# Performance work log

Measured on AMD Instinct MI355X. Metric: run time of the kernel, lower is better.

The kernel has to match this reference:

```python
import jax, jax.numpy as jnp
import numpy as np

D_MODEL = 1024
N_HEADS = 16
HEAD_DIM = D_MODEL // N_HEADS
WINDOW = 256


def setup_inputs() -> dict:
    key = jax.random.key(0)
    kx, kq, ko = jax.random.split(key, 3)
    B, T = 4, 2048
    x = jax.random.normal(kx, (B, T, D_MODEL), dtype=jnp.float32)
    s = 1.0 / np.sqrt(D_MODEL)
    w_qkv = jax.random.normal(kq, (D_MODEL, 3 * D_MODEL), dtype=jnp.float32) * s
    w_out = jax.random.normal(ko, (D_MODEL, D_MODEL), dtype=jnp.float32) * s
    return {"x": x, "w_qkv": w_qkv, "w_out": w_out}


def reference(x, w_qkv, w_out):
    B, T, C = x.shape
    qkv = (x @ w_qkv).reshape(B, T, 3, N_HEADS, HEAD_DIM)
    q, k, v = qkv[:, :, 0], qkv[:, :, 1], qkv[:, :, 2]  # [B,T,H,D]
    # sliding-window causal mask: position i attends to j in (i-W, i]
    i = jnp.arange(T)[:, None]
    j = jnp.arange(T)[None, :]
    allowed = (j <= i) & (j > i - WINDOW)
    mask = jnp.where(allowed, 0.0, -jnp.inf).astype(x.dtype)  # [T,T]
    scale = 1.0 / np.sqrt(HEAD_DIM)
    scores = jnp.einsum('bqhd,bkhd->bhqk', q, k) * scale + mask
    attn = jax.nn.softmax(scores, axis=-1)
    out = jnp.einsum('bhqk,bkhd->bqhd', attn, v).reshape(B, T, C)
    return out @ w_out
```

## Files before the change

kernel.cpp:

```cpp
#include <hip/hip_runtime.h>

typedef unsigned short u16;
typedef __attribute__((ext_vector_type(8))) short bh8;
typedef __attribute__((ext_vector_type(4))) float f4;
typedef __attribute__((ext_vector_type(4))) unsigned short us4;

#define T_SEQ 2048
#define NHEADS 16
#define DHEAD 64
#define WIN 256

#define MF(a, b, c) __builtin_amdgcn_mfma_f32_16x16x32_bf16((a), (b), (c), 0, 0, 0)

__device__ __forceinline__ float bf2f(u16 u) {
  union { unsigned int i; float f; } v; v.i = ((unsigned int)u) << 16; return v.f;
}
__device__ __forceinline__ u16 f2bf(float f) {
  unsigned int u = __float_as_uint(f);
  u = u + 0x7fffu + ((u >> 16) & 1u);
  return (u16)(u >> 16);
}
__device__ __forceinline__ void async16(const void* g, void* l) {
  void* gv = const_cast<void*>(g);
  __builtin_amdgcn_global_load_lds(
      (__attribute__((address_space(1))) void*)gv,
      (__attribute__((address_space(3))) void*)l, 16, 0, 0);
}

__device__ __forceinline__ int is_f32_probe(const void* x) {
  const float* xf = (const float*)x;
  const int lane = threadIdx.x & 63;
  int bad = 0;
  #pragma unroll
  for (int u = 0; u < 4; ++u) {
    const float v = xf[lane * 4 + u];
    const float a = fabsf(v);
    bad |= (!(a < 64.f)) || (!(v == 0.f || a > 1e-30f));
  }
  return __any(bad) ? 0 : 1;
}

__global__ __launch_bounds__(256) void prep(
    const void* __restrict__ x, const void* __restrict__ w_qkv,
    const void* __restrict__ w_out, u16* __restrict__ xbf,
    u16* __restrict__ wqkvT, u16* __restrict__ woutT, int have_x)
{
  const int bid = blockIdx.x;
  const int tid = threadIdx.x;
  const int isf = is_f32_probe(x);

  if (bid < 4096) {
    if (!have_x) return;
    const size_t e = ((size_t)bid * 256 + tid) * 8;
    if (isf) {
      const float* f = (const float*)x;
      us4 o0, o1;
      #pragma unroll
      for (int u = 0; u < 4; ++u) { o0[u] = f2bf(f[e + u]); o1[u] = f2bf(f[e + 4 + u]); }
      *(us4*)&xbf[e] = o0; *(us4*)&xbf[e + 4] = o1;
    } else {
      *(us4*)&xbf[e]     = *(const us4*)&((const u16*)x)[e];
      *(us4*)&xbf[e + 4] = *(const us4*)&((const u16*)x)[e + 4];
    }
  } else {
    __shared__ alignas(16) u16 tile[32][33];
    const void* in; u16* out; int C, bx, by;
    const int t0 = bid - 4096;
    if (t0 < 3072) { in = w_qkv; out = wqkvT; C = 3072; bx = t0 % 96; by = t0 / 96; }
    else           { const int t = t0 - 3072; in = w_out; out = woutT; C = 1024; bx = t % 32; by = t / 32; }
    const int tx4 = (tid & 7) * 4;
    const int iy  = tid >> 3;
    const int y0 = by * 32;
    if (isf) {
      f4 v = *(const f4*)&((const float*)in)[(size_t)(y0 + iy) * C + bx * 32 + tx4];
      #pragma unroll
      for (int u = 0; u < 4; ++u) tile[iy][tx4 + u] = f2bf(v[u]);
    } else {
      us4 v = *(const us4*)&((const u16*)in)[(size_t)(y0 + iy) * C + bx * 32 + tx4];
      #pragma unroll
      for (int u = 0; u < 4; ++u) tile[iy][tx4 + u] = v[u];
    }
    __syncthreads();
    const int i2 = tid >> 3;
    us4 o;
    #pragma unroll
    for (int u = 0; u < 4; ++u) o[u] = tile[tx4 + u][i2];
    *(us4*)&out[(size_t)(bx * 32 + i2) * 1024 + y0 + tx4] = o;
  }
}

template<int BN, bool ADYN, bool CDYN>
__global__ __launch_bounds__(256, 4) void gemm_bt(
    const void* __restrict__ A, const u16* __restrict__ Bt,
    void* __restrict__ C, int N, int K, int lda, int ldc,
    const void* __restrict__ xprobe)
{
  constexpr int NJ = BN / 32;
  __shared__ alignas(16) u16 As[128 * 64];
  __shared__ alignas(16) u16 Bs[BN * 64];

  const int isf  = (ADYN || CDYN) ? is_f32_probe(xprobe) : 0;
  const int tid  = threadIdx.x;
  const int lane = tid & 63;
  const int w    = tid >> 6;
  const int wm   = (w >> 1) * 64;
  const int wn   = (w & 1) * (BN / 2);
  const int quad = lane >> 4;
  const int l16  = lane & 15;
  const int row0 = blockIdx.y * 128;
  const int col0 = blockIdx.x * BN;

  f4 acc[4][NJ] = {};

  size_t aoff[4]; const u16* bsrc[NJ]; int lofs[4];
  #pragma unroll
  for (int s = 0; s < 4; ++s) {
    const int r  = s * 32 + (tid >> 3);
    const int gc = (tid & 7) ^ (r & 7);
    aoff[s] = (size_t)(row0 + r) * lda + gc * 8;
    lofs[s] = s * 4096 + tid * 16;
  }
  #pragma unroll
  for (int s = 0; s < NJ; ++s) {
    const int r  = s * 32 + (tid >> 3);
    const int gc = (tid & 7) ^ (r & 7);
    bsrc[s] = Bt + (size_t)(col0 + r) * K + gc * 8;
  }

  const bool af32 = ADYN && isf;

  for (int k0 = 0; k0 < K; k0 += 64) {
    if (af32) {
      const float* Af = (const float*)A;
      bh8 a[4];
      #pragma unroll
      for (int s = 0; s < 4; ++s) {
        f4 u0 = *(const f4*)(Af + aoff[s] + k0);
        f4 u1 = *(const f4*)(Af + aoff[s] + k0 + 4);
        #pragma unroll
        for (int u = 0; u < 4; ++u) { a[s][u] = (short)f2bf(u0[u]); a[s][u + 4] = (short)f2bf(u1[u]); }
      }
      __syncthreads();
      #pragma unroll
      for (int s = 0; s < 4; ++s)
        *(bh8*)((char*)As + lofs[s]) = a[s];
      #pragma unroll
      for (int s = 0; s < NJ; ++s)
        async16(bsrc[s] + k0, (char*)Bs + lofs[s]);
    } else {
      const u16* A16 = (const u16*)A;
      __syncthreads();
      #pragma unroll
      for (int s = 0; s < 4; ++s)
        async16(A16 + aoff[s] + k0, (char*)As + lofs[s]);
      #pragma unroll
      for (int s = 0; s < NJ; ++s)
        async16(bsrc[s] + k0, (char*)Bs + lofs[s]);
    }
    __builtin_amdgcn_s_waitcnt(0);
    __syncthreads();

    #pragma unroll
    for (int ks = 0; ks < 2; ++ks) {
      bh8 af[4], bf[NJ];
      #pragma unroll
      for (int i = 0; i < 4; ++i) {
        const int row = wm + i * 16 + l16;
        const int lc  = (ks * 4 + quad) ^ (row & 7);
        af[i] = *(const bh8*)(As + row * 64 + lc * 8);
      }
      #pragma unroll
      for (int j = 0; j < NJ; ++j) {
        const int row = wn + j * 16 + l16;
        const int lc  = (ks * 4 + quad) ^ (row & 7);
        bf[j] = *(const bh8*)(Bs + row * 64 + lc * 8);
      }
      #pragma unroll
      for (int i = 0; i < 4; ++i)
        #pragma unroll
        for (int j = 0; j < NJ; ++j)
          acc[i][j] = MF(af[i], bf[j], acc[i][j]);
    }
  }

  const bool cf32 = CDYN && isf;
  #pragma unroll
  for (int i = 0; i < 4; ++i) {
    #pragma unroll
    for (int j = 0; j < NJ; ++j) {
      const int rb = row0 + wm + i * 16 + quad * 4;
      const int cc = col0 + wn + j * 16 + l16;
      #pragma unroll
      for (int r = 0; r < 4; ++r) {
        if (cf32) ((float*)C)[(size_t)(rb + r) * ldc + cc] = acc[i][j][r];
        else      ((u16*)C)[(size_t)(rb + r) * ldc + cc]   = f2bf(acc[i][j][r]);
      }
    }
  }
}

__global__ __launch_bounds__(256) void attn_mfma(const u16* __restrict__ qkv,
                                                 u16* __restrict__ att, int ldo)
{
  __shared__ alignas(16) u16 Kt[64 * 72];
  __shared__ alignas(16) u16 Vt[64 * 72];
  __shared__ alignas(16) u16 Ps[64 * 72];

  const int tid  = threadIdx.x;
  const int lane = tid & 63;
  const int w    = tid >> 6;
  const int quad = lane >> 4;
  const int l16  = lane & 15;
  const int qb = blockIdx.x, h = blockIdx.y, b = blockIdx.z;
  const int qs = qb * 64;

  const u16* base = qkv + (size_t)b * T_SEQ * 3072 + h * 64;

  const size_t qrowg = (size_t)(qs + w * 16 + l16) * 3072;
  bh8 qa0 = *(const bh8*)&base[qrowg + quad * 8];
  bh8 qa1 = *(const bh8*)&base[qrowg + 32 + quad * 8];
  #pragma unroll
  for (int u = 0; u < 8; ++u) {
    qa0[u] = (short)f2bf(bf2f((u16)qa0[u]) * 0.125f);
    qa1[u] = (short)f2bf(bf2f((u16)qa1[u]) * 0.125f);
  }

  f4 Oc[4] = {};
  float mst[4] = {-1e30f, -1e30f, -1e30f, -1e30f};
  float lst[4] = {0.f, 0.f, 0.f, 0.f};

  const int tmin = (qb >= 4) ? 0 : (4 - qb);
  const int c8  = (tid & 7) * 8;
  const int r0s = tid >> 3;

  for (int t = tmin; t < 5; ++t) {
    const int kt0 = qs - 256 + t * 64;
    const bool diag  = (t == 4);
    const bool ledge = (t == 0);
    const int kb_lo = ledge ? w : 0;
    const int kb_hi = diag  ? w : 3;
    __syncthreads();

    #pragma unroll
    for (int r = r0s; r < 64; r += 32) {
      *(bh8*)&Kt[r * 72 + c8] =
          *(const bh8*)&base[(size_t)(kt0 + r) * 3072 + 1024 + c8];
      bh8 v = *(const bh8*)&base[(size_t)(kt0 + r) * 3072 + 2048 + c8];
      const int kc = r >> 3, ki = r & 7;
      #pragma unroll
      for (int u = 0; u < 8; ++u) {
        const int d = c8 + u;
        Vt[d * 72 + ((kc ^ (d >> 3)) << 3) + ki] = (u16)v[u];
      }
    }
    __syncthreads();

    f4 S[4];
    #pragma unroll
    for (int kb = 0; kb < 4; ++kb) {
      if (kb < kb_lo || kb > kb_hi) {
        S[kb][0] = S[kb][1] = S[kb][2] = S[kb][3] = -1e30f;
      } else {
        const int krow = (kb * 16 + l16) * 72;
        bh8 kf0 = *(const bh8*)&Kt[krow + quad * 8];
        bh8 kf1 = *(const bh8*)&Kt[krow + 32 + quad * 8];
        f4 s = {};
        s = MF(qa0, kf0, s);
        s = MF(qa1, kf1, s);
        S[kb] = s;
      }
    }

    if (diag || ledge) {
      #pragma unroll
      for (int kb = 0; kb < 4; ++kb) {
        if (kb == w) {
          #pragma unroll
          for (int rr = 0; rr < 4; ++rr) {
            const int ii = quad * 4 + rr;
            const bool ok = diag ? (l16 <= ii) : (l16 > ii);
            if (!ok) S[kb][rr] = -1e30f;
          }
        }
      }
    }

    float tmax[4] = {-1e30f, -1e30f, -1e30f, -1e30f};
    #pragma unroll
    for (int kb = 0; kb < 4; ++kb)
      #pragma unroll
      for (int rr = 0; rr < 4; ++rr)
        tmax[rr] = fmaxf(tmax[rr], S[kb][rr]);
    #pragma unroll
    for (int off = 1; off < 16; off <<= 1)
      #pragma unroll
      for (int rr = 0; rr < 4; ++rr)
        tmax[rr] = fmaxf(tmax[rr], __shfl_xor(tmax[rr], off));

    const bool grew = (tmax[0] > mst[0] + 8.f) || (tmax[1] > mst[1] + 8.f) ||
                      (tmax[2] > mst[2] + 8.f) || (tmax[3] > mst[3] + 8.f);
    if (__any(grew)) {
      #pragma unroll
      for (int rr = 0; rr < 4; ++rr) {
        const float mnew = fmaxf(mst[rr], tmax[rr]);
        const float al = __expf(mst[rr] - mnew);
        mst[rr] = mnew;
        lst[rr] *= al;
        #pragma unroll
        for (int db = 0; db < 4; ++db) Oc[db][rr] *= al;
      }
    }

    float rsum[4] = {0.f, 0.f, 0.f, 0.f};
    const int swq = quad >> 1;
    #pragma unroll
    for (int kb = 0; kb < 4; ++kb) {
      const int kc = kb * 2 + (l16 >> 3);
      const int ki = l16 & 7;
      #pragma unroll
      for (int rr = 0; rr < 4; ++rr) {
        const float p = __expf(S[kb][rr] - mst[rr]);
        rsum[rr] += p;
        const int q = w * 16 + quad * 4 + rr;
        Ps[q * 72 + ((kc ^ swq) << 3) + ki] = f2bf(p);
      }
    }
    #pragma unroll
    for (int off = 1; off < 16; off <<= 1)
      #pragma unroll
      for (int rr = 0; rr < 4; ++rr)
        rsum[rr] += __shfl_xor(rsum[rr], off);
    #pragma unroll
    for (int rr = 0; rr < 4; ++rr)
      lst[rr] += rsum[rr];

    {
      const int q = w * 16 + l16;
      const int swp = (q >> 3) & 1;
      bh8 pa0 = *(const bh8*)&Ps[q * 72 + (((0 + quad) ^ swp) << 3)];
      bh8 pa1 = *(const bh8*)&Ps[q * 72 + (((4 + quad) ^ swp) << 3)];
      #pragma unroll
      for (int db = 0; db < 4; ++db) {
        const int d = db * 16 + l16;
        const int dsw = d >> 3;
        bh8 vb0 = *(const bh8*)&Vt[d * 72 + (((0 + quad) ^ dsw) << 3)];
        bh8 vb1 = *(const bh8*)&Vt[d * 72 + (((4 + quad) ^ dsw) << 3)];
        Oc[db] = MF(pa0, vb0, Oc[db]);
        Oc[db] = MF(pa1, vb1, Oc[db]);
      }
    }
  }

  u16* obase = att + (size_t)b * T_SEQ * ldo + h * 64;
  #pragma unroll
  for (int rr = 0; rr < 4; ++rr) {
    const int i = qs + w * 16 + quad * 4 + rr;
    const float inv = 1.f / lst[rr];
    #pragma unroll
    for (int db = 0; db < 4; ++db)
      obase[(size_t)i * ldo + db * 16 + l16] = f2bf(Oc[db][rr] * inv);
  }
}

extern "C" void kernel_launch(void* const* d_in, const int* in_sizes, int n_in,
                              void* d_out, int out_size, void* d_ws, size_t ws_size,
                              hipStream_t stream) {
  const void* x     = d_in[0];
  const void* w_qkv = d_in[1];
  const void* w_out = d_in[2];

  const size_t SZ_QKV = (size_t)8192 * 3072 * 2;
  const size_t SZ_XBF = (size_t)8192 * 1024 * 2;
  const size_t SZ_WQ  = (size_t)3072 * 1024 * 2;
  const size_t SZ_WO  = (size_t)1024 * 1024 * 2;
  const size_t SZ_ATT = (size_t)8192 * 1024 * 2;

  char* p = (char*)d_ws;
  u16* qkv   = (u16*)p; p += SZ_QKV;
  u16* wqkvT = (u16*)p; p += SZ_WQ;
  u16* woutT = (u16*)p; p += SZ_WO;
  u16* xbf   = (u16*)p; p += SZ_XBF;
  u16* attb  = (u16*)p;
  const size_t need_x   = SZ_QKV + SZ_WQ + SZ_WO + SZ_XBF;
  const bool have_x   = ws_size >= need_x;
  const bool have_att = ws_size >= need_x + SZ_ATT;

  prep<<<dim3(8192), 256, 0, stream>>>(x, w_qkv, w_out, xbf, wqkvT, woutT,
                                       have_x ? 1 : 0);

  if (have_x) {
    gemm_bt<128, false, false><<<dim3(24, 64), 256, 0, stream>>>(
        xbf, wqkvT, qkv, 3072, 1024, 1024, 3072, x);
  } else {
    gemm_bt<128, true, false><<<dim3(24, 64), 256, 0, stream>>>(
        x, wqkvT, qkv, 3072, 1024, 1024, 3072, x);
  }

  u16* attp  = have_att ? attb : qkv;
  const int ldo = have_att ? 1024 : 3072;
  attn_mfma<<<dim3(32, NHEADS, 4), 256, 0, stream>>>(qkv, attp, ldo);

  gemm_bt<64, false, true><<<dim3(16, 64), 256, 0, stream>>>(
      attp, woutT, d_out, 1024, 1024, ldo, 1024, x);
}
```

Baseline: 223.6 us.

## Double-buffer K tiles with async LDS loads and prefetch V in attention

The attention kernel now prefetches the next K tile directly into a double-buffered, XOR-swizzled shared-memory array using global_load_lds. The next V rows are loaded into registers during the current iteration, so global load latency overlaps with the MFMA and softmax work. It also reuses the xbf workspace buffer for the attention output instead of needing a separate allocation. The cost is more register pressure and manual vmcnt waits, which must match the number of outstanding loads to stay correct.

Result: faster. 218.9 us (-2.1%).

```diff
diff --git a/kernel.cpp b/kernel.cpp
--- a/kernel.cpp
+++ b/kernel.cpp
@@ -11,6 +11,7 @@
 #define WIN 256
 
 #define MF(a, b, c) __builtin_amdgcn_mfma_f32_16x16x32_bf16((a), (b), (c), 0, 0, 0)
+#define VMCNT(n) asm volatile("s_waitcnt vmcnt(" #n ")" ::: "memory")
 
 __device__ __forceinline__ float bf2f(u16 u) {
   union { unsigned int i; float f; } v; v.i = ((unsigned int)u) << 16; return v.f;
@@ -202,7 +203,7 @@
 __global__ __launch_bounds__(256) void attn_mfma(const u16* __restrict__ qkv,
                                                  u16* __restrict__ att, int ldo)
 {
-  __shared__ alignas(16) u16 Kt[64 * 72];
+  __shared__ alignas(16) u16 Kt[2][64 * 64];
   __shared__ alignas(16) u16 Vt[64 * 72];
   __shared__ alignas(16) u16 Ps[64 * 72];
 
@@ -216,6 +217,15 @@
 
   const u16* base = qkv + (size_t)b * T_SEQ * 3072 + h * 64;
 
+  const int r0 = tid >> 3;
+  const int r1 = 32 + r0;
+  const int c0 = tid & 7;
+  const int gc0 = c0 ^ (r0 & 7);
+  const int gc1 = c0 ^ (r1 & 7);
+  const int c8  = c0 * 8;
+
+  const int tmin = (qb >= 4) ? 0 : (4 - qb);
+
   const size_t qrowg = (size_t)(qs + w * 16 + l16) * 3072;
   bh8 qa0 = *(const bh8*)&base[qrowg + quad * 8];
   bh8 qa1 = *(const bh8*)&base[qrowg + 32 + quad * 8];
@@ -225,13 +235,21 @@
     qa1[u] = (short)f2bf(bf2f((u16)qa1[u]) * 0.125f);
   }
 
+  {
+    const int kt0 = qs - 256 + tmin * 64;
+    async16(&base[(size_t)(kt0 + r0) * 3072 + 1024 + gc0 * 8], (char*)Kt[tmin & 1] + tid * 16);
+    async16(&base[(size_t)(kt0 + r1) * 3072 + 1024 + gc1 * 8], (char*)Kt[tmin & 1] + 4096 + tid * 16);
+  }
+  bh8 vr0, vr1;
+  {
+    const int kt0 = qs - 256 + tmin * 64;
+    vr0 = *(const bh8*)&base[(size_t)(kt0 + r0) * 3072 + 2048 + c8];
+    vr1 = *(const bh8*)&base[(size_t)(kt0 + r1) * 3072 + 2048 + c8];
+  }
+
   f4 Oc[4] = {};
   float mst[4] = {-1e30f, -1e30f, -1e30f, -1e30f};
   float lst[4] = {0.f, 0.f, 0.f, 0.f};
-
-  const int tmin = (qb >= 4) ? 0 : (4 - qb);
-  const int c8  = (tid & 7) * 8;
-  const int r0s = tid >> 3;
 
   for (int t = tmin; t < 5; ++t) {
     const int kt0 = qs - 256 + t * 64;
@@ -239,31 +257,41 @@
     const bool ledge = (t == 0);
     const int kb_lo = ledge ? w : 0;
     const int kb_hi = diag  ? w : 3;
+    const bool more = (t + 1) < 5;
+
+    bh8 vn0, vn1;
+    if (more) {
+      const int kn0 = kt0 + 64;
+      async16(&base[(size_t)(kn0 + r0) * 3072 + 1024 + gc0 * 8], (char*)Kt[(t + 1) & 1] + tid * 16);
+      async16(&base[(size_t)(kn0 + r1) * 3072 + 1024 + gc1 * 8], (char*)Kt[(t + 1) & 1] + 4096 + tid * 16);
+      vn0 = *(const bh8*)&base[(size_t)(kn0 + r0) * 3072 + 2048 + c8];
+      vn1 = *(const bh8*)&base[(size_t)(kn0 + r1) * 3072 + 2048 + c8];
+    }
+    if (more) { VMCNT(4); } else { VMCNT(0); }
     __syncthreads();
 
-    #pragma unroll
-    for (int r = r0s; r < 64; r += 32) {
-      *(bh8*)&Kt[r * 72 + c8] =
-          *(const bh8*)&base[(size_t)(kt0 + r) * 3072 + 1024 + c8];
-      bh8 v = *(const bh8*)&base[(size_t)(kt0 + r) * 3072 + 2048 + c8];
-      const int kc = r >> 3, ki = r & 7;
+    {
+      const int kc0 = r0 >> 3, ki0 = r0 & 7;
+      const int kc1 = r1 >> 3, ki1 = r1 & 7;
       #pragma unroll
       for (int u = 0; u < 8; ++u) {
         const int d = c8 + u;
-        Vt[d * 72 + ((kc ^ (d >> 3)) << 3) + ki] = (u16)v[u];
+        Vt[d * 72 + ((kc0 ^ (d >> 3)) << 3) + ki0] = (u16)vr0[u];
+        Vt[d * 72 + ((kc1 ^ (d >> 3)) << 3) + ki1] = (u16)vr1[u];
       }
     }
     __syncthreads();
 
+    const u16* Kb = Kt[t & 1];
     f4 S[4];
     #pragma unroll
     for (int kb = 0; kb < 4; ++kb) {
       if (kb < kb_lo || kb > kb_hi) {
         S[kb][0] = S[kb][1] = S[kb][2] = S[kb][3] = -1e30f;
       } else {
-        const int krow = (kb * 16 + l16) * 72;
-        bh8 kf0 = *(const bh8*)&Kt[krow + quad * 8];
-        bh8 kf1 = *(const bh8*)&Kt[krow + 32 + quad * 8];
+        const int row = kb * 16 + l16;
+        bh8 kf0 = *(const bh8*)&Kb[row * 64 + (((quad    ) ^ (row & 7)) << 3)];
+        bh8 kf1 = *(const bh8*)&Kb[row * 64 + (((quad + 4) ^ (row & 7)) << 3)];
         f4 s = {};
         s = MF(qa0, kf0, s);
         s = MF(qa1, kf1, s);
@@ -349,6 +377,7 @@
         Oc[db] = MF(pa1, vb1, Oc[db]);
       }
     }
+    vr0 = vn0; vr1 = vn1;
   }
 
   u16* obase = att + (size_t)b * T_SEQ * ldo + h * 64;
@@ -373,17 +402,14 @@
   const size_t SZ_XBF = (size_t)8192 * 1024 * 2;
   const size_t SZ_WQ  = (size_t)3072 * 1024 * 2;
   const size_t SZ_WO  = (size_t)1024 * 1024 * 2;
-  const size_t SZ_ATT = (size_t)8192 * 1024 * 2;
 
   char* p = (char*)d_ws;
   u16* qkv   = (u16*)p; p += SZ_QKV;
   u16* wqkvT = (u16*)p; p += SZ_WQ;
   u16* woutT = (u16*)p; p += SZ_WO;
   u16* xbf   = (u16*)p; p += SZ_XBF;
-  u16* attb  = (u16*)p;
-  const size_t need_x   = SZ_QKV + SZ_WQ + SZ_WO + SZ_XBF;
+  const size_t need_x = SZ_QKV + SZ_WQ + SZ_WO + SZ_XBF;
   const bool have_x   = ws_size >= need_x;
-  const bool have_att = ws_size >= need_x + SZ_ATT;
 
   prep<<<dim3(8192), 256, 0, stream>>>(x, w_qkv, w_out, xbf, wqkvT, woutT,
                                        have_x ? 1 : 0);
@@ -396,8 +422,8 @@
         x, wqkvT, qkv, 3072, 1024, 1024, 3072, x);
   }
 
-  u16* attp  = have_att ? attb : qkv;
-  const int ldo = have_att ? 1024 : 3072;
+  u16* attp  = have_x ? xbf : qkv;
+  const int ldo = have_x ? 1024 : 3072;
   attn_mfma<<<dim3(32, NHEADS, 4), 256, 0, stream>>>(qkv, attp, ldo);
 
   gemm_bt<64, false, true><<<dim3(16, 64), 256, 0, stream>>>(
```
